# Optimization experiments

Hardware: AMD Instinct MI355X
Metric: run time of the kernel (lower is better)

Reference implementation:

```python
import jax, jax.numpy as jnp
import numpy as np

C = 512
GROUPS = 32
EPS = 1e-6

def setup_inputs() -> dict:
    key = jax.random.key(0)
    ks = jax.random.split(key, 6)
    s = 1.0 / np.sqrt(C)
    return {
        "x": jax.random.normal(ks[0], (2, C, 16, 32, 32), dtype=jnp.float32),
        "gamma": jnp.ones((C,), jnp.float32),
        "beta": jnp.zeros((C,), jnp.float32),
        "q_w": jax.random.normal(ks[1], (C, C), jnp.float32) * s,
        "q_b": jnp.zeros((C,), jnp.float32),
        "k_w": jax.random.normal(ks[2], (C, C), jnp.float32) * s,
        "k_b": jnp.zeros((C,), jnp.float32),
        "v_w": jax.random.normal(ks[3], (C, C), jnp.float32) * s,
        "v_b": jnp.zeros((C,), jnp.float32),
        "proj_w": jax.random.normal(ks[4], (C, C), jnp.float32) * s,
        "proj_b": jnp.zeros((C,), jnp.float32),
    }

def _group_norm(x, gamma, beta):
    # x: [b, c, t, h, w]
    b, c, t, h, w = x.shape
    xg = x.reshape(b, GROUPS, c // GROUPS, t, h, w)
    mean = xg.mean(axis=(2, 3, 4, 5), keepdims=True)
    var = xg.var(axis=(2, 3, 4, 5), keepdims=True)
    xg = (xg - mean) * jax.lax.rsqrt(var + EPS)
    x = xg.reshape(b, c, t, h, w)
    return x * gamma[None, :, None, None, None] + beta[None, :, None, None, None]

def _pw_conv(x, w, bias):
    # 1x1x1 conv == channel GEMM. x: [b,c,t,h,w], w: [c_out, c_in]
    y = jnp.einsum('bcthw,oc->bothw', x, w)
    return y + bias[None, :, None, None, None]

def reference(x, gamma, beta, q_w, q_b, k_w, k_b, v_w, v_b, proj_w, proj_b):
    b, c, t, h, w = x.shape
    hn = _group_norm(x, gamma, beta)
    q = _pw_conv(hn, q_w, q_b)
    k = _pw_conv(hn, k_w, k_b)
    v = _pw_conv(hn, v_w, v_b)
    # [b,c,t,h,w] -> [b*t, h*w, c]
    def to_seq(a):
        return jnp.transpose(a, (0, 2, 3, 4, 1)).reshape(b * t, h * w, c)
    q, k, v = to_seq(q), to_seq(k), to_seq(v)
    scale = 1.0 / jnp.sqrt(jnp.asarray(c, x.dtype))
    attn = jnp.einsum('bqc,bkc->bqk', q, k) * scale  # [b*t, hw, hw]
    attn = jax.nn.softmax(attn, axis=-1)
    out = jnp.einsum('bqk,bkc->bqc', attn, v)
    out = out.reshape(b, t, h, w, c).transpose(0, 4, 1, 2, 3)
    return x + _pw_conv(out, proj_w, proj_b)
```

## Files before the change

kernel.cpp:

```cpp
#include <hip/hip_runtime.h>

typedef unsigned short u16;
typedef __attribute__((ext_vector_type(8))) short bf16x8;
typedef __attribute__((ext_vector_type(4))) float f32x4;

#define DEV static __device__ __forceinline__

DEV u16 f2bf(float f) {
  union { float f; unsigned u; } x; x.f = f;
  return (u16)((x.u + 0x7FFFu + ((x.u >> 16) & 1u)) >> 16);
}
DEV float bf2f(u16 h) { union { unsigned u; float f; } x; x.u = ((unsigned)h) << 16; return x.f; }

DEV void gload16(const void* g, void* l) {
  __builtin_amdgcn_global_load_lds((const __attribute__((address_space(1))) void*)g,
                                   (__attribute__((address_space(3))) void*)l, 16, 0, 0);
}

__global__ __launch_bounds__(256) void gn_stats_a(const float* __restrict__ x,
                                                  float2* __restrict__ part) {
  const int bg = blockIdx.x >> 5, slice = blockIdx.x & 31;
  const float* base = x + (long)bg * 262144 + slice * 8192;
  float s = 0.f, q = 0.f;
#pragma unroll
  for (int i = 0; i < 8; ++i) {
    float4 v = *(const float4*)(base + i * 1024 + threadIdx.x * 4);
    s += v.x + v.y + v.z + v.w;
    q += v.x * v.x + v.y * v.y + v.z * v.z + v.w * v.w;
  }
#pragma unroll
  for (int o = 32; o; o >>= 1) { s += __shfl_xor(s, o); q += __shfl_xor(q, o); }
  __shared__ float2 red[4];
  if ((threadIdx.x & 63) == 0) red[threadIdx.x >> 6] = make_float2(s, q);
  __syncthreads();
  if (threadIdx.x == 0) {
    float S = 0.f, Q = 0.f;
    for (int i = 0; i < 4; ++i) { S += red[i].x; Q += red[i].y; }
    part[blockIdx.x] = make_float2(S, Q);
  }
}

__global__ void gn_stats_b(const float2* __restrict__ part, float2* __restrict__ stats) {
  float s = 0.f, q = 0.f;
  if (threadIdx.x < 32) {
    float2 p = part[blockIdx.x * 32 + threadIdx.x];
    s = p.x; q = p.y;
  }
#pragma unroll
  for (int o = 32; o; o >>= 1) { s += __shfl_xor(s, o); q += __shfl_xor(q, o); }
  if (threadIdx.x == 0) {
    const float inv = 1.f / 262144.f;
    float mean = s * inv;
    float var = q * inv - mean * mean;
    stats[blockIdx.x] = make_float2(mean, rsqrtf(var + 1e-6f));
  }
}

__global__ __launch_bounds__(256) void gn_apply(const float* __restrict__ x,
                                                const float* __restrict__ gamma,
                                                const float* __restrict__ beta,
                                                const float2* __restrict__ stats,
                                                u16* __restrict__ hn) {
  __shared__ u16 tile[64][65];
  const int p0 = blockIdx.x * 64, c0 = blockIdx.y * 64, bt = blockIdx.z;
  const int b = bt >> 4, t = bt & 15, tid = threadIdx.x;
  const float* xb = x + (long)b * 8388608 + t * 1024;
#pragma unroll 4
  for (int r = 0; r < 16; ++r) {
    int ci = r * 4 + (tid >> 6), pi = tid & 63;
    int c = c0 + ci;
    float2 st = stats[b * 32 + (c >> 4)];
    float v = xb[(long)c * 16384 + p0 + pi];
    v = (v - st.x) * st.y * gamma[c] + beta[c];
    tile[ci][pi] = f2bf(v);
  }
  __syncthreads();
  u16* hb = hn + ((long)bt * 1024 + p0) * 512 + c0;
#pragma unroll 4
  for (int r = 0; r < 16; ++r) {
    int pi = r * 4 + (tid >> 6), ci = tid & 63;
    hb[(long)pi * 512 + ci] = tile[ci][pi];
  }
}

__global__ __launch_bounds__(256) void wconv(const float* __restrict__ w0, const float* __restrict__ w1,
                                             const float* __restrict__ w2, const float* __restrict__ w3,
                                             u16* __restrict__ dst) {
  int e = (blockIdx.x * 256 + threadIdx.x) * 4;
  const float* src = w0;
  int which = e >> 18, off = e & 262143;
  if (which == 1) src = w1; else if (which == 2) src = w2; else if (which == 3) src = w3;
  float4 v = *(const float4*)(src + off);
  ushort4 o;
  o.x = f2bf(v.x); o.y = f2bf(v.y); o.z = f2bf(v.z); o.w = f2bf(v.w);
  *(ushort4*)(dst + e) = o;
}

__global__ void bcat(const float* __restrict__ qb, const float* __restrict__ kb,
                     const float* __restrict__ vb, float* __restrict__ dst) {
  int i = blockIdx.x * 256 + threadIdx.x;
  if (i < 512) dst[i] = qb[i];
  else if (i < 1024) dst[i] = kb[i - 512];
  else if (i < 1536) dst[i] = vb[i - 1024];
}

__global__ __launch_bounds__(256) void transpose_pc(const u16* __restrict__ v, int ldv,
                                                    u16* __restrict__ vT) {
  __shared__ u16 tile[64][65];
  const int p0 = blockIdx.x * 64, c0 = blockIdx.y * 64;
  const long bt = blockIdx.z;
  const int tid = threadIdx.x;
  const u16* vb = v + bt * 1024 * (long)ldv;
#pragma unroll 4
  for (int r = 0; r < 16; ++r) {
    int pi = r * 4 + (tid >> 6), ci = tid & 63;
    tile[pi][ci] = vb[(long)(p0 + pi) * ldv + c0 + ci];
  }
  __syncthreads();
  u16* ob = vT + bt * 524288;
#pragma unroll 4
  for (int r = 0; r < 16; ++r) {
    int ci = r * 4 + (tid >> 6), pi = tid & 63;
    ob[(long)(c0 + ci) * 1024 + p0 + pi] = tile[pi][ci];
  }
}

__global__ __launch_bounds__(256) void softmax_rows_bf16(u16* __restrict__ scores) {
  const int wave = threadIdx.x >> 6, lane = threadIdx.x & 63;
  const long row = (long)blockIdx.x * 4 + wave;
  u16* srow = scores + row * 1024;
  bf16x8 a0 = *(const bf16x8*)(srow + lane * 16);
  bf16x8 a1 = *(const bf16x8*)(srow + lane * 16 + 8);
  float v[16];
#pragma unroll
  for (int j = 0; j < 8; ++j) { v[j] = bf2f((u16)a0[j]); v[8 + j] = bf2f((u16)a1[j]); }
  float m = v[0];
#pragma unroll
  for (int j = 1; j < 16; ++j) m = fmaxf(m, v[j]);
#pragma unroll
  for (int o = 32; o; o >>= 1) m = fmaxf(m, __shfl_xor(m, o));
  const float sc = 0.044194173824159216f;
  float s = 0.f, e[16];
#pragma unroll
  for (int j = 0; j < 16; ++j) { e[j] = __expf((v[j] - m) * sc); s += e[j]; }
#pragma unroll
  for (int o = 32; o; o >>= 1) s += __shfl_xor(s, o);
  const float inv = 1.f / s;
  bf16x8 o0, o1;
#pragma unroll
  for (int j = 0; j < 8; ++j) {
    o0[j] = (short)f2bf(e[j] * inv);
    o1[j] = (short)f2bf(e[8 + j] * inv);
  }
  *(bf16x8*)(srow + lane * 16) = o0;
  *(bf16x8*)(srow + lane * 16 + 8) = o1;
}

#define SYNC_MID() do { asm volatile("" ::: "memory"); __builtin_amdgcn_s_barrier(); \
  asm volatile("s_waitcnt lgkmcnt(0)" ::: "memory"); __builtin_amdgcn_sched_barrier(0); } while (0)
#define SYNC_END() do { asm volatile("" ::: "memory"); __builtin_amdgcn_s_barrier(); \
  asm volatile("" ::: "memory"); } while (0)

template <bool OUT_BF16, bool HAS_BIAS>
__global__ __launch_bounds__(512, 2) void gemm8p(
    const u16* __restrict__ A, int lda, long sA,
    const u16* __restrict__ B, int ldb, long sB,
    void* __restrict__ Cv, int ldc, long sC,
    const float* __restrict__ bias, int K) {
  __shared__ u16 sm[2 * 32768];
  const int tid = threadIdx.x;
  const int wid = tid >> 6, lane = tid & 63;
  const int wm = wid >> 2, wn = wid & 3;

  int bx = blockIdx.x, by = blockIdx.y;
  if (gridDim.z == 1 && (((int)gridDim.x * (int)gridDim.y) & 7) == 0) {
    int gy = gridDim.y;
    int d = by * gridDim.x + bx;
    int per = ((int)gridDim.x * gy) >> 3;
    int w = (d & 7) * per + (d >> 3);
    bx = w / gy; by = w % gy;
  }
  const long m0 = (long)bx * 256;
  const long n0 = (long)by * 256;
  A += (long)blockIdx.z * sA + m0 * lda;
  B += (long)blockIdx.z * sB + n0 * ldb;
  const int NT = K >> 6;

  f32x4 acc[8][4] = {};

  char* smc = (char*)sm;
  auto STAGE_HALF = [&](int kt, int which) {
    const char* src = (const char*)((which < 2) ? A : B);
    const long ldby = 2L * ((which < 2) ? lda : ldb);
    const int rowbase = (which & 1) * 128;
    char* dst = smc + (kt & 1) * 65536 + ((which < 2) ? 0 : 32768) + rowbase * 128;
    const char* gk = src + (long)kt * 128;
#pragma unroll
    for (int i = 0; i < 2; ++i) {
      int rl = i * 64 + (tid >> 3);
      int cb = (tid & 7) * 16;
      int scb = cb ^ ((rl & 7) << 4);
      gload16(gk + (long)(rowbase + rl) * ldby + scb, dst + rl * 128 + cb);
    }
  };

  const int lrow = lane & 15, kslot = (lane >> 4) * 16;
  auto RD_A = [&](int buf, int kk, int mh, bf16x8* af) {
#pragma unroll
    for (int mi = 0; mi < 4; ++mi) {
      int row = wm * 128 + (mh * 4 + mi) * 16 + lrow;
      int cb = (kk * 64 + kslot) ^ ((row & 7) << 4);
      af[mi] = *(const bf16x8*)(smc + buf * 65536 + row * 128 + cb);
    }
  };
  auto RD_B = [&](int buf, int kk, bf16x8* bf) {
#pragma unroll
    for (int ni = 0; ni < 4; ++ni) {
      int row = wn * 64 + ni * 16 + lrow;
      int cb = (kk * 64 + kslot) ^ ((row & 7) << 4);
      bf[ni] = *(const bf16x8*)(smc + buf * 65536 + 32768 + row * 128 + cb);
    }
  };

  STAGE_HALF(0, 0); STAGE_HALF(0, 1); STAGE_HALF(0, 2); STAGE_HALF(0, 3);
  if (NT > 1) { STAGE_HALF(1, 2); STAGE_HALF(1, 3); }
  asm volatile("s_waitcnt vmcnt(4)" ::: "memory");
  SYNC_END();

  for (int T = 0; T < NT; ++T) {
    const int cur = T & 1;
    const bool s1 = (T + 1 < NT), s2 = (T + 2 < NT);
    bf16x8 af[4], bf[4];
    RD_B(cur, 0, bf);
    RD_A(cur, 0, 0, af);
    if (s1) STAGE_HALF(T + 1, 0);
    SYNC_MID();
    __builtin_amdgcn_s_setprio(1);
#pragma unroll
    for (int mi = 0; mi < 4; ++mi)
#pragma unroll
      for (int ni = 0; ni < 4; ++ni)
        acc[mi][ni] = __builtin_amdgcn_mfma_f32_16x16x32_bf16(af[mi], bf[ni], acc[mi][ni], 0, 0, 0);
    __builtin_amdgcn_s_setprio(0);
    SYNC_END();
    RD_A(cur, 0, 1, af);
    if (s1) STAGE_HALF(T + 1, 1);
    SYNC_MID();
    __builtin_amdgcn_s_setprio(1);
#pragma unroll
    for (int mi = 0; mi < 4; ++mi)
#pragma unroll
      for (int ni = 0; ni < 4; ++ni)
        acc[4 + mi][ni] = __builtin_amdgcn_mfma_f32_16x16x32_bf16(af[mi], bf[ni], acc[4 + mi][ni], 0, 0, 0);
    __builtin_amdgcn_s_setprio(0);
    SYNC_END();
    RD_B(cur, 1, bf);
    RD_A(cur, 1, 0, af);
    SYNC_MID();
    __builtin_amdgcn_s_setprio(1);
#pragma unroll
    for (int mi = 0; mi < 4; ++mi)
#pragma unroll
      for (int ni = 0; ni < 4; ++ni)
        acc[mi][ni] = __builtin_amdgcn_mfma_f32_16x16x32_bf16(af[mi], bf[ni], acc[mi][ni], 0, 0, 0);
    __builtin_amdgcn_s_setprio(0);
    SYNC_END();
    RD_A(cur, 1, 1, af);
    if (s2) { STAGE_HALF(T + 2, 2); STAGE_HALF(T + 2, 3); }
    SYNC_MID();
    __builtin_amdgcn_s_setprio(1);
#pragma unroll
    for (int mi = 0; mi < 4; ++mi)
#pragma unroll
      for (int ni = 0; ni < 4; ++ni)
        acc[4 + mi][ni] = __builtin_amdgcn_mfma_f32_16x16x32_bf16(af[mi], bf[ni], acc[4 + mi][ni], 0, 0, 0);
    __builtin_amdgcn_s_setprio(0);
    if (s2) asm volatile("s_waitcnt vmcnt(4)" ::: "memory");
    else    asm volatile("s_waitcnt vmcnt(0)" ::: "memory");
    SYNC_END();
  }

  const int lc = lane & 15, lr = (lane >> 4) * 4;
  if (OUT_BF16) {
    u16* C = (u16*)Cv + (long)blockIdx.z * sC;
#pragma unroll
    for (int mi = 0; mi < 8; ++mi) {
      long r = m0 + wm * 128 + mi * 16 + lr;
#pragma unroll
      for (int ni = 0; ni < 4; ++ni) {
        long c = n0 + wn * 64 + ni * 16 + lc;
        float bv = HAS_BIAS ? bias[c] : 0.f;
#pragma unroll
        for (int j = 0; j < 4; ++j) C[(r + j) * ldc + c] = f2bf(acc[mi][ni][j] + bv);
      }
    }
  } else {
    float* C = (float*)Cv + (long)blockIdx.z * sC;
#pragma unroll
    for (int mi = 0; mi < 8; ++mi) {
      long r = m0 + wm * 128 + mi * 16 + lr;
#pragma unroll
      for (int ni = 0; ni < 4; ++ni) {
        long c = n0 + wn * 64 + ni * 16 + lc;
        float bv = HAS_BIAS ? bias[c] : 0.f;
#pragma unroll
        for (int j = 0; j < 4; ++j) C[(r + j) * ldc + c] = acc[mi][ni][j] + bv;
      }
    }
  }
}

__global__ __launch_bounds__(256) void final_write(const float* __restrict__ projout,
                                                   const float* __restrict__ proj_b,
                                                   const float* __restrict__ x,
                                                   float* __restrict__ out) {
  __shared__ float tile[64][65];
  const int p0 = blockIdx.x * 64, c0 = blockIdx.y * 64, bt = blockIdx.z;
  const int b = bt >> 4, t = bt & 15, tid = threadIdx.x;
  const float* pr = projout + ((long)bt * 1024 + p0) * 512 + c0;
#pragma unroll 4
  for (int r = 0; r < 16; ++r) {
    int pi = r * 4 + (tid >> 6), ci = tid & 63;
    tile[pi][ci] = pr[(long)pi * 512 + ci];
  }
  __syncthreads();
  const long obase = (long)b * 8388608 + t * 1024;
#pragma unroll 4
  for (int r = 0; r < 16; ++r) {
    int ci = r * 4 + (tid >> 6), pi = tid & 63;
    long idx = obase + (long)(c0 + ci) * 16384 + p0 + pi;
    out[idx] = x[idx] + proj_b[c0 + ci] + tile[pi][ci];
  }
}

extern "C" void kernel_launch(void* const* d_in, const int* in_sizes, int n_in,
                              void* d_out, int out_size, void* d_ws, size_t ws_size,
                              hipStream_t stream) {
  (void)in_sizes; (void)n_in; (void)out_size;
  const float* x      = (const float*)d_in[0];
  const float* gamma  = (const float*)d_in[1];
  const float* beta   = (const float*)d_in[2];
  const float* q_w    = (const float*)d_in[3];
  const float* q_b    = (const float*)d_in[4];
  const float* k_w    = (const float*)d_in[5];
  const float* k_b    = (const float*)d_in[6];
  const float* v_w    = (const float*)d_in[7];
  const float* v_b    = (const float*)d_in[8];
  const float* proj_w = (const float*)d_in[9];
  const float* proj_b = (const float*)d_in[10];

  const size_t OFF_WB    = 0;
  const size_t OFF_BIAS  = 2097152;
  const size_t OFF_STATS = 2103296;
  const size_t OFF_PART  = 2103808;
  const size_t OFF_HN    = 2121728;
  const size_t OFF_QKV   = 35676160;
  const size_t OFF_SC    = 136339456;

  char* ws = (char*)d_ws;
  u16*    wb      = (u16*)(ws + OFF_WB);
  float*  qkvbias = (float*)(ws + OFF_BIAS);
  float2* stats   = (float2*)(ws + OFF_STATS);
  float2* part    = (float2*)(ws + OFF_PART);
  u16*    hn      = (u16*)(ws + OFF_HN);
  u16*    vT      = hn;
  u16*    qkv     = (u16*)(ws + OFF_QKV);
  float*  projout = (float*)(ws + OFF_QKV);
  u16*    scores  = (u16*)(ws + OFF_SC);

  const int CH = (ws_size >= 237002752ULL) ? 32 : 8;
  u16* ob = (u16*)(ws + OFF_SC + (size_t)CH * 2097152);

  wconv<<<1024, 256, 0, stream>>>(q_w, k_w, v_w, proj_w, wb);
  bcat<<<6, 256, 0, stream>>>(q_b, k_b, v_b, qkvbias);
  gn_stats_a<<<2048, 256, 0, stream>>>(x, part);
  gn_stats_b<<<64, 64, 0, stream>>>(part, stats);
  gn_apply<<<dim3(16, 8, 32), 256, 0, stream>>>(x, gamma, beta, stats, hn);

  gemm8p<true, true><<<dim3(128, 6, 1), 512, 0, stream>>>(
      hn, 512, 0, wb, 512, 0, qkv, 1536, 0, qkvbias, 512);

  transpose_pc<<<dim3(16, 8, 32), 256, 0, stream>>>(qkv + 1024, 1536, vT);

  for (int ch = 0; ch < 32 / CH; ++ch) {
    long f0 = (long)ch * CH;
    gemm8p<true, false><<<dim3(4, 4, CH), 512, 0, stream>>>(
        qkv + f0 * 1572864, 1536, 1572864,
        qkv + 512 + f0 * 1572864, 1536, 1572864,
        scores, 1024, 1048576, nullptr, 512);
    softmax_rows_bf16<<<CH * 256, 256, 0, stream>>>(scores);
    gemm8p<true, false><<<dim3(4, 2, CH), 512, 0, stream>>>(
        scores, 1024, 1048576,
        vT + f0 * 524288, 1024, 524288,
        ob + f0 * 524288, 512, 524288, nullptr, 1024);
  }

  gemm8p<false, false><<<dim3(128, 2, 1), 512, 0, stream>>>(
      ob, 512, 0, wb + 786432, 512, 0, projout, 512, 0, nullptr, 512);
  final_write<<<dim3(16, 8, 32), 256, 0, stream>>>(projout, proj_b, x, (float*)d_out);
}
```

Baseline: 309.1 us.

## Precompute GEMM load addresses, swizzle batched grids, store projection output as bf16

The GEMM main loop now works from precomputed global and LDS pointer offsets that are advanced or XOR-toggled each iteration, replacing the per-call lambda address math. The XCD-aware block remapping now also covers batched (z>1) launches, so the attention GEMMs get the same spread of blocks across dies. The projection GEMM writes bf16 instead of fp32, roughly halving its write traffic and the read traffic in final_write, at the cost of an extra bf16 rounding step before the residual add.

```diff
diff --git a/kernel.cpp b/kernel.cpp
--- a/kernel.cpp
+++ b/kernel.cpp
@@ -168,121 +168,118 @@
     void* __restrict__ Cv, int ldc, long sC,
     const float* __restrict__ bias, int K) {
   __shared__ u16 sm[2 * 32768];
+  char* smc = (char*)sm;
   const int tid = threadIdx.x;
   const int wid = tid >> 6, lane = tid & 63;
   const int wm = wid >> 2, wn = wid & 3;
 
-  int bx = blockIdx.x, by = blockIdx.y;
-  if (gridDim.z == 1 && (((int)gridDim.x * (int)gridDim.y) & 7) == 0) {
-    int gy = gridDim.y;
-    int d = by * gridDim.x + bx;
-    int per = ((int)gridDim.x * gy) >> 3;
-    int w = (d & 7) * per + (d >> 3);
-    bx = w / gy; by = w % gy;
-  }
-  const long m0 = (long)bx * 256;
-  const long n0 = (long)by * 256;
-  A += (long)blockIdx.z * sA + m0 * lda;
-  B += (long)blockIdx.z * sB + n0 * ldb;
+  int bx = blockIdx.x, by = blockIdx.y, bz = blockIdx.z;
+  {
+    unsigned gx = gridDim.x, gy = gridDim.y;
+    unsigned total = gx * gy * gridDim.z;
+    if ((total & 7u) == 0) {
+      unsigned gxy = gx * gy;
+      unsigned d = (blockIdx.z * gy + blockIdx.y) * gx + blockIdx.x;
+      unsigned w = (d & 7u) * (total >> 3) + (d >> 3);
+      bz = w / gxy; unsigned r = w - (unsigned)bz * gxy;
+      bx = r / gy;  by = r - (unsigned)bx * gy;
+    }
+  }
+  const long m0 = (long)bx * 256, n0 = (long)by * 256;
+  const char* Ab = (const char*)(A + (long)bz * sA + m0 * lda);
+  const char* Bb = (const char*)(B + (long)bz * sB + n0 * ldb);
   const int NT = K >> 6;
+  const long lda2 = 2L * lda, ldb2 = 2L * ldb;
+
+  const int r8 = tid >> 3;
+  const int sw2 = (r8 & 7) << 4;
+  const int cb0 = ((tid & 7) * 16) ^ sw2;
+  const int dB = r8 * 128 + (tid & 7) * 16;
+  const char* gA00 = Ab + (long)(r8      ) * lda2 + cb0;
+  const char* gA01 = Ab + (long)(r8 +  64) * lda2 + cb0;
+  const char* gA10 = Ab + (long)(r8 + 128) * lda2 + cb0;
+  const char* gA11 = Ab + (long)(r8 + 192) * lda2 + cb0;
+  const char* gB00 = Bb + (long)(r8      ) * ldb2 + cb0;
+  const char* gB01 = Bb + (long)(r8 +  64) * ldb2 + cb0;
+  const char* gB10 = Bb + (long)(r8 + 128) * ldb2 + cb0;
+  const char* gB11 = Bb + (long)(r8 + 192) * ldb2 + cb0;
+
+  const int lrow = lane & 15, kslot = (lane >> 4) * 16;
+  const int sw = (lrow & 7) << 4;
+  int a0 = (wm * 128 + lrow) * 128 + (kslot ^ sw);
+  int a1 = a0 ^ 64;
+  int b0 = 32768 + (wn * 64 + lrow) * 128 + (kslot ^ sw);
+  int b1 = b0 ^ 64;
 
   f32x4 acc[8][4] = {};
 
-  char* smc = (char*)sm;
-  auto STAGE_HALF = [&](int kt, int which) {
-    const char* src = (const char*)((which < 2) ? A : B);
-    const long ldby = 2L * ((which < 2) ? lda : ldb);
-    const int rowbase = (which & 1) * 128;
-    char* dst = smc + (kt & 1) * 65536 + ((which < 2) ? 0 : 32768) + rowbase * 128;
-    const char* gk = src + (long)kt * 128;
-#pragma unroll
-    for (int i = 0; i < 2; ++i) {
-      int rl = i * 64 + (tid >> 3);
-      int cb = (tid & 7) * 16;
-      int scb = cb ^ ((rl & 7) << 4);
-      gload16(gk + (long)(rowbase + rl) * ldby + scb, dst + rl * 128 + cb);
-    }
-  };
-
-  const int lrow = lane & 15, kslot = (lane >> 4) * 16;
-  auto RD_A = [&](int buf, int kk, int mh, bf16x8* af) {
-#pragma unroll
-    for (int mi = 0; mi < 4; ++mi) {
-      int row = wm * 128 + (mh * 4 + mi) * 16 + lrow;
-      int cb = (kk * 64 + kslot) ^ ((row & 7) << 4);
-      af[mi] = *(const bf16x8*)(smc + buf * 65536 + row * 128 + cb);
-    }
-  };
-  auto RD_B = [&](int buf, int kk, bf16x8* bf) {
-#pragma unroll
-    for (int ni = 0; ni < 4; ++ni) {
-      int row = wn * 64 + ni * 16 + lrow;
-      int cb = (kk * 64 + kslot) ^ ((row & 7) << 4);
-      bf[ni] = *(const bf16x8*)(smc + buf * 65536 + 32768 + row * 128 + cb);
-    }
-  };
-
-  STAGE_HALF(0, 0); STAGE_HALF(0, 1); STAGE_HALF(0, 2); STAGE_HALF(0, 3);
-  if (NT > 1) { STAGE_HALF(1, 2); STAGE_HALF(1, 3); }
+#define STG(p, dof, bufbit) gload16((p), smc + ((bufbit) << 16) + (dof))
+#define RD4(dst, off) do { \
+    dst[0] = *(const bf16x8*)(smc + (off));          \
+    dst[1] = *(const bf16x8*)(smc + (off) + 2048);   \
+    dst[2] = *(const bf16x8*)(smc + (off) + 4096);   \
+    dst[3] = *(const bf16x8*)(smc + (off) + 6144);   \
+  } while (0)
+#define MFMA16(ah, bh, accb) do { \
+    __builtin_amdgcn_s_setprio(1); \
+    _Pragma("unroll") \
+    for (int mi = 0; mi < 4; ++mi) \
+      _Pragma("unroll") \
+      for (int ni = 0; ni < 4; ++ni) \
+        acc[(accb) + mi][ni] = __builtin_amdgcn_mfma_f32_16x16x32_bf16(ah[mi], bh[ni], acc[(accb) + mi][ni], 0, 0, 0); \
+    __builtin_amdgcn_s_setprio(0); \
+  } while (0)
+
+  STG(gA00, dB, 0);         STG(gA01, dB + 8192, 0);
+  STG(gA10, dB + 16384, 0); STG(gA11, dB + 24576, 0);
+  STG(gB00, dB + 32768, 0); STG(gB01, dB + 40960, 0);
+  STG(gB10, dB + 49152, 0); STG(gB11, dB + 57344, 0);
+  STG(gB00 + 128, dB + 32768, 1); STG(gB01 + 128, dB + 40960, 1);
+  STG(gB10 + 128, dB + 49152, 1); STG(gB11 + 128, dB + 57344, 1);
+  gA00 += 128; gA01 += 128; gA10 += 128; gA11 += 128;
+  gB00 += 256; gB01 += 256; gB10 += 256; gB11 += 256;
   asm volatile("s_waitcnt vmcnt(4)" ::: "memory");
   SYNC_END();
 
   for (int T = 0; T < NT; ++T) {
-    const int cur = T & 1;
+    const int cur = T & 1, nxt = cur ^ 1;
     const bool s1 = (T + 1 < NT), s2 = (T + 2 < NT);
     bf16x8 af[4], bf[4];
-    RD_B(cur, 0, bf);
-    RD_A(cur, 0, 0, af);
-    if (s1) STAGE_HALF(T + 1, 0);
+    RD4(bf, b0);
+    RD4(af, a0);
+    if (s1) { STG(gA00, dB, nxt); STG(gA01, dB + 8192, nxt); }
     SYNC_MID();
-    __builtin_amdgcn_s_setprio(1);
-#pragma unroll
-    for (int mi = 0; mi < 4; ++mi)
-#pragma unroll
-      for (int ni = 0; ni < 4; ++ni)
-        acc[mi][ni] = __builtin_amdgcn_mfma_f32_16x16x32_bf16(af[mi], bf[ni], acc[mi][ni], 0, 0, 0);
-    __builtin_amdgcn_s_setprio(0);
+    MFMA16(af, bf, 0);
     SYNC_END();
-    RD_A(cur, 0, 1, af);
-    if (s1) STAGE_HALF(T + 1, 1);
+    RD4(af, a0 + 8192);
+    if (s1) { STG(gA10, dB + 16384, nxt); STG(gA11, dB + 24576, nxt); }
     SYNC_MID();
-    __builtin_amdgcn_s_setprio(1);
-#pragma unroll
-    for (int mi = 0; mi < 4; ++mi)
-#pragma unroll
-      for (int ni = 0; ni < 4; ++ni)
-        acc[4 + mi][ni] = __builtin_amdgcn_mfma_f32_16x16x32_bf16(af[mi], bf[ni], acc[4 + mi][ni], 0, 0, 0);
-    __builtin_amdgcn_s_setprio(0);
+    MFMA16(af, bf, 4);
     SYNC_END();
-    RD_B(cur, 1, bf);
-    RD_A(cur, 1, 0, af);
+    RD4(bf, b1);
+    RD4(af, a1);
     SYNC_MID();
-    __builtin_amdgcn_s_setprio(1);
-#pragma unroll
-    for (int mi = 0; mi < 4; ++mi)
-#pragma unroll
-      for (int ni = 0; ni < 4; ++ni)
-        acc[mi][ni] = __builtin_amdgcn_mfma_f32_16x16x32_bf16(af[mi], bf[ni], acc[mi][ni], 0, 0, 0);
-    __builtin_amdgcn_s_setprio(0);
+    MFMA16(af, bf, 0);
     SYNC_END();
-    RD_A(cur, 1, 1, af);
-    if (s2) { STAGE_HALF(T + 2, 2); STAGE_HALF(T + 2, 3); }
+    RD4(af, a1 + 8192);
+    if (s2) { STG(gB00, dB + 32768, cur); STG(gB01, dB + 40960, cur);
+              STG(gB10, dB + 49152, cur); STG(gB11, dB + 57344, cur); }
     SYNC_MID();
-    __builtin_amdgcn_s_setprio(1);
-#pragma unroll
-    for (int mi = 0; mi < 4; ++mi)
-#pragma unroll
-      for (int ni = 0; ni < 4; ++ni)
-        acc[4 + mi][ni] = __builtin_amdgcn_mfma_f32_16x16x32_bf16(af[mi], bf[ni], acc[4 + mi][ni], 0, 0, 0);
-    __builtin_amdgcn_s_setprio(0);
+    MFMA16(af, bf, 4);
     if (s2) asm volatile("s_waitcnt vmcnt(4)" ::: "memory");
     else    asm volatile("s_waitcnt vmcnt(0)" ::: "memory");
     SYNC_END();
-  }
+    gA00 += 128; gA01 += 128; gA10 += 128; gA11 += 128;
+    gB00 += 128; gB01 += 128; gB10 += 128; gB11 += 128;
+    a0 ^= 65536; a1 ^= 65536; b0 ^= 65536; b1 ^= 65536;
+  }
+#undef STG
+#undef RD4
+#undef MFMA16
 
   const int lc = lane & 15, lr = (lane >> 4) * 4;
   if (OUT_BF16) {
-    u16* C = (u16*)Cv + (long)blockIdx.z * sC;
+    u16* C = (u16*)Cv + (long)bz * sC;
 #pragma unroll
     for (int mi = 0; mi < 8; ++mi) {
       long r = m0 + wm * 128 + mi * 16 + lr;
@@ -295,7 +292,7 @@
       }
     }
   } else {
-    float* C = (float*)Cv + (long)blockIdx.z * sC;
+    float* C = (float*)Cv + (long)bz * sC;
 #pragma unroll
     for (int mi = 0; mi < 8; ++mi) {
       long r = m0 + wm * 128 + mi * 16 + lr;
@@ -310,18 +307,18 @@
   }
 }
 
-__global__ __launch_bounds__(256) void final_write(const float* __restrict__ projout,
+__global__ __launch_bounds__(256) void final_write(const u16* __restrict__ projout,
                                                    const float* __restrict__ proj_b,
                                                    const float* __restrict__ x,
                                                    float* __restrict__ out) {
   __shared__ float tile[64][65];
   const int p0 = blockIdx.x * 64, c0 = blockIdx.y * 64, bt = blockIdx.z;
   const int b = bt >> 4, t = bt & 15, tid = threadIdx.x;
-  const float* pr = projout + ((long)bt * 1024 + p0) * 512 + c0;
+  const u16* pr = projout + ((long)bt * 1024 + p0) * 512 + c0;
 #pragma unroll 4
   for (int r = 0; r < 16; ++r) {
     int pi = r * 4 + (tid >> 6), ci = tid & 63;
-    tile[pi][ci] = pr[(long)pi * 512 + ci];
+    tile[pi][ci] = bf2f(pr[(long)pi * 512 + ci]);
   }
   __syncthreads();
   const long obase = (long)b * 8388608 + t * 1024;
@@ -365,7 +362,7 @@
   u16*    hn      = (u16*)(ws + OFF_HN);
   u16*    vT      = hn;
   u16*    qkv     = (u16*)(ws + OFF_QKV);
-  float*  projout = (float*)(ws + OFF_QKV);
+  u16*    projout = (u16*)(ws + OFF_QKV);
   u16*    scores  = (u16*)(ws + OFF_SC);
 
   const int CH = (ws_size >= 237002752ULL) ? 32 : 8;
@@ -395,7 +392,7 @@
         ob + f0 * 524288, 512, 524288, nullptr, 1024);
   }
 
-  gemm8p<false, false><<<dim3(128, 2, 1), 512, 0, stream>>>(
+  gemm8p<true, false><<<dim3(128, 2, 1), 512, 0, stream>>>(
       ob, 512, 0, wb + 786432, 512, 0, projout, 512, 0, nullptr, 512);
   final_write<<<dim3(16, 8, 32), 256, 0, stream>>>(projout, proj_b, x, (float*)d_out);
 }
```

Result: faster. 284.3 us (-8.0%).
